# Kernel tuning notes

Measured on AMD Instinct MI355X. Metric: run time of the kernel, lower is better.

## Reference

```python
import jax, jax.numpy as jnp
import numpy as np

B, U, V, C = 2, 8, 512, 256
H, DK = 8, 64            # num_heads, key_query_features (per head)
R = 256                  # result_features; per-head value dim R//H = 32
CODE = 192
EPS = 1e-6               # affinity renorm epsilon
LN_EPS = 1e-5            # torch LayerNorm default
GAIN = 2.5               # post_attention_gain / post_mlp_gain buffers


def _ln(x, g, b):
    m = x.mean(-1, keepdims=True)
    v = ((x - m) ** 2).mean(-1, keepdims=True)
    return (x - m) / jnp.sqrt(v + LN_EPS) * g + b


def _modlin(x, c, W, Wc, b=None):
    # ModFC / ModLin: y = W(x * (1 + Wc c)) (+ b)
    y = (x * (1.0 + c @ Wc)) @ W
    return y if b is None else y + b


def setup_inputs() -> dict:
    key = jax.random.key(0)
    ks = jax.random.split(key, 16)
    s = 0.02
    return {
        'variables': jax.random.normal(ks[0], (B, U, V, C), jnp.float32),
        'codes': jax.random.normal(ks[1], (U, CODE), jnp.float32),
        'affinities': jax.random.uniform(ks[2], (B, U, V), jnp.float32),
        'ln1_g': jnp.ones((C,), jnp.float32),
        'ln1_b': jnp.zeros((C,), jnp.float32),
        'Wq': jax.random.normal(ks[3], (C, H * DK), jnp.float32) * s,
        'Wcq': jax.random.normal(ks[4], (CODE, C), jnp.float32) * s,
        'Wk': jax.random.normal(ks[5], (C, H * DK), jnp.float32) * s,
        'Wck': jax.random.normal(ks[6], (CODE, C), jnp.float32) * s,
        'Wv': jax.random.normal(ks[7], (C, R), jnp.float32) * s,
        'Wcv': jax.random.normal(ks[8], (CODE, C), jnp.float32) * s,
        'bv': jnp.zeros((R,), jnp.float32),
        'ln2_g': jnp.ones((R,), jnp.float32),
        'ln2_b': jnp.zeros((R,), jnp.float32),
        'W1': jax.random.normal(ks[9], (R, R), jnp.float32) * s,
        'Wc1': jax.random.normal(ks[10], (CODE, R), jnp.float32) * s,
        'b1m': jnp.zeros((R,), jnp.float32),
        'W2': jax.random.normal(ks[11], (R, R), jnp.float32) * s,
        'Wc2': jax.random.normal(ks[12], (CODE, R), jnp.float32) * s,
        'b2m': jnp.zeros((R,), jnp.float32),
    }


def reference(variables, codes, affinities, ln1_g, ln1_b, Wq, Wcq, Wk, Wck,
              Wv, Wcv, bv, ln2_g, ln2_b, W1, Wc1, b1m, W2, Wc2, b2m):
    # codes: [U, code] -> broadcast to [B, U, V, code]
    c4 = jnp.broadcast_to(codes[None, :, None, :], (B, U, V, CODE))
    xn = _ln(variables, ln1_g, ln1_b)                      # b u v c
    q = _modlin(xn, c4, Wq, Wcq).reshape(B, U, V, H, DK)   # b u v h d
    k = _modlin(xn, c4, Wk, Wck).reshape(B, U, V, H, DK)
    v = _modlin(xn, c4, Wv, Wcv, bv).reshape(B, U, V, H, R // H)
    # scores: b u r s h (attention over s); scale_attention_weights=False -> scale 1
    scores = jnp.einsum('burhd,bushd->bursh', q, k)
    dot = jax.nn.softmax(scores, axis=3)                   # softmax over s (dim=-2)
    # affinity modulation: aff_r * aff_s * weights, renormalized over s
    kmw = affinities[:, :, :, None, None] * affinities[:, :, None, :, None] * dot
    kmw = kmw / (kmw.sum(axis=3, keepdims=True) + EPS)
    att = jnp.einsum('bursh,bushc->burhc', kmw, v).reshape(B, U, V, R)
    g = affinities[..., None]
    # residual_mode='gating', variable_features==result_features
    attn_out = (1.0 - g) * variables + g * GAIN * att
    yn = _ln(attn_out, ln2_g, ln2_b)
    h1 = jax.nn.gelu(_modlin(yn, c4, W1, Wc1, b1m), approximate=False)
    h2 = jax.nn.gelu(_modlin(h1, c4, W2, Wc2, b2m), approximate=False)
    mlp_out = h2 * g
    results = (1.0 - g) * attn_out + g * GAIN * mlp_out
    return results
```

## Files before the change

kernel.cpp:

```cpp
#include <hip/hip_runtime.h>
#include <math.h>

#define B_ 2
#define U_ 8
#define V_ 512
#define C_ 256
#define H_ 8
#define R_ 256
#define EPS_ 1e-6f
#define LN_EPS_ 1e-5f
#define GAIN_ 2.5f

typedef __attribute__((ext_vector_type(8))) short bf16x8;
typedef __attribute__((ext_vector_type(4))) float f32x4;
typedef unsigned short ushort_t;

__device__ __forceinline__ ushort_t f2bf(float x) {
    union { float f; unsigned u; } v; v.f = x;
    unsigned r = v.u + 0x7fffu + ((v.u >> 16) & 1u);
    return (ushort_t)(r >> 16);
}

__device__ __forceinline__ float waveReduceSum(float v) {
    #pragma unroll
    for (int m = 1; m < 64; m <<= 1) v += __shfl_xor(v, m);
    return v;
}

__device__ __forceinline__ float gelu_exact(float x) {
    return 0.5f * x * (1.f + erff(x * 0.70710678118654752f));
}

__global__ __launch_bounds__(256) void k_prep(
    const float* __restrict__ codes,
    const float* __restrict__ Wcq, const float* __restrict__ Wck,
    const float* __restrict__ Wcv, const float* __restrict__ Wc1,
    const float* __restrict__ Wc2,
    const float* __restrict__ Wq, const float* __restrict__ Wk,
    const float* __restrict__ Wv, const float* __restrict__ W1,
    const float* __restrict__ W2,
    const float* __restrict__ x, const float* __restrict__ ln1g,
    const float* __restrict__ ln1b,
    ushort_t* __restrict__ wqkvT, ushort_t* __restrict__ w1T,
    ushort_t* __restrict__ w2T, ushort_t* __restrict__ xnb) {
    int bid = blockIdx.x;
    int tid = threadIdx.x;
    if (bid >= 896) {
        int row = (bid - 896) * 4 + (tid >> 6);
        int lane = tid & 63;
        const float* xr = x + (size_t)row * C_;
        float4 v = *(const float4*)&xr[lane * 4];
        float s = v.x + v.y + v.z + v.w;
        float ss = v.x * v.x + v.y * v.y + v.z * v.z + v.w * v.w;
        s = waveReduceSum(s); ss = waveReduceSum(ss);
        float mean = s * (1.f / 256.f);
        float var = ss * (1.f / 256.f) - mean * mean;
        float rstd = rsqrtf(var + LN_EPS_);
        float4 gg = *(const float4*)&ln1g[lane * 4];
        float4 bb = *(const float4*)&ln1b[lane * 4];
        unsigned lo = (unsigned)f2bf((v.x - mean) * rstd * gg.x + bb.x)
                    | ((unsigned)f2bf((v.y - mean) * rstd * gg.y + bb.y) << 16);
        unsigned hi = (unsigned)f2bf((v.z - mean) * rstd * gg.z + bb.z)
                    | ((unsigned)f2bf((v.w - mean) * rstd * gg.w + bb.w) << 16);
        uint2 pk; pk.x = lo; pk.y = hi;
        *(uint2*)&xnb[(size_t)row * C_ + lane * 4] = pk;
        return;
    }
    __shared__ float mpart[4][64];
    __shared__ float mrow[64];
    __shared__ ushort_t T[64][65];
    int id = bid;
    const float* W; int ldw, modIdx, colAdd, tilesPerU, base;
    ushort_t* dst; int dstCols;
    if (id < 256)      { base = 0;   W = Wq; ldw = 512; modIdx = 0; colAdd = 0;    dst = wqkvT; dstCols = 1280; tilesPerU = 32; }
    else if (id < 512) { base = 256; W = Wk; ldw = 512; modIdx = 1; colAdd = 512;  dst = wqkvT; dstCols = 1280; tilesPerU = 32; }
    else if (id < 640) { base = 512; W = Wv; ldw = 256; modIdx = 2; colAdd = 1024; dst = wqkvT; dstCols = 1280; tilesPerU = 16; }
    else if (id < 768) { base = 640; W = W1; ldw = 256; modIdx = 3; colAdd = 0;    dst = w1T;  dstCols = 256;  tilesPerU = 16; }
    else               { base = 768; W = W2; ldw = 256; modIdx = 4; colAdd = 0;    dst = w2T;  dstCols = 256;  tilesPerU = 16; }
    const float* Wc = (modIdx == 0) ? Wcq : (modIdx == 1) ? Wck :
                      (modIdx == 2) ? Wcv : (modIdx == 3) ? Wc1 : Wc2;
    int local = id - base;
    int u = local / tilesPerU;
    int t = local % tilesPerU;
    int nColTiles = ldw / 64;
    int c0 = (t / nColTiles) * 64;
    int col0 = (t % nColTiles) * 64;
    {
        const float* cd = codes + u * 192;
        int cc = tid & 63, g = tid >> 6;
        float accm = 0.f;
        #pragma unroll 4
        for (int jj = 0; jj < 48; ++jj) {
            int j = g * 48 + jj;
            accm = fmaf(cd[j], Wc[j * 256 + c0 + cc], accm);
        }
        mpart[g][cc] = accm;
        __syncthreads();
        if (tid < 64)
            mrow[tid] = 1.f + mpart[0][tid] + mpart[1][tid] + mpart[2][tid] + mpart[3][tid];
        __syncthreads();
    }
    int cl = tid >> 4;
    int cg = (tid & 15) * 4;
    #pragma unroll
    for (int it = 0; it < 4; ++it) {
        int c = cl + it * 16;
        float m = mrow[c];
        float4 wv = *(const float4*)&W[(size_t)(c0 + c) * ldw + col0 + cg];
        T[c][cg + 0] = f2bf(wv.x * m);
        T[c][cg + 1] = f2bf(wv.y * m);
        T[c][cg + 2] = f2bf(wv.z * m);
        T[c][cg + 3] = f2bf(wv.w * m);
    }
    __syncthreads();
    int j = tid >> 2;
    int ch = (tid & 3) * 16;
    ushort_t tmp[16];
    #pragma unroll
    for (int i = 0; i < 16; ++i) tmp[i] = T[ch + i][j];
    ushort_t* o = dst + ((size_t)u * dstCols + colAdd + col0 + j) * 256 + c0 + ch;
    *(bf16x8*)&o[0] = *(const bf16x8*)&tmp[0];
    *(bf16x8*)&o[8] = *(const bf16x8*)&tmp[8];
}

__global__ __launch_bounds__(256) void k_qkv(
    const ushort_t* __restrict__ X, const ushort_t* __restrict__ WT,
    const float* __restrict__ bv, ushort_t* __restrict__ out,
    ushort_t* __restrict__ vT) {
    __shared__ __align__(16) ushort_t xs[128][72];
    __shared__ __align__(16) ushort_t wt[128][72];
    int col0 = blockIdx.x * 128;
    int row0 = blockIdx.y * 128;
    int u = (row0 >> 9) & 7;
    const ushort_t* Wu = WT + (size_t)(u * 1280 + col0) * 256;
    int tid = threadIdx.x;
    int w = tid >> 6, l = tid & 63;
    int lr = l & 15, lg = l >> 4;
    int wm = w >> 1, wn = w & 1;
    f32x4 acc[4][4] = {};
    int sr = tid >> 3, sko = (tid & 7) * 8;
    for (int k0 = 0; k0 < 256; k0 += 64) {
        #pragma unroll
        for (int it = 0; it < 4; ++it) {
            int r = sr + it * 32;
            *(bf16x8*)&xs[r][sko] = *(const bf16x8*)&X[(size_t)(row0 + r) * 256 + k0 + sko];
            *(bf16x8*)&wt[r][sko] = *(const bf16x8*)&Wu[(size_t)r * 256 + k0 + sko];
        }
        __syncthreads();
        #pragma unroll
        for (int m = 0; m < 4; ++m) {
            #pragma unroll
            for (int kk = 0; kk < 2; ++kk) {
                bf16x8 a = *(const bf16x8*)&xs[wm * 64 + m * 16 + lr][kk * 32 + lg * 8];
                #pragma unroll
                for (int n = 0; n < 4; ++n) {
                    bf16x8 bb = *(const bf16x8*)&wt[wn * 64 + n * 16 + lr][kk * 32 + lg * 8];
                    acc[m][n] = __builtin_amdgcn_mfma_f32_16x16x32_bf16(a, bb, acc[m][n], 0, 0, 0);
                }
            }
        }
        __syncthreads();
    }
    #pragma unroll
    for (int m = 0; m < 4; ++m) {
        int rowb = row0 + wm * 64 + m * 16 + lg * 4;
        #pragma unroll
        for (int n = 0; n < 4; ++n) {
            int col = col0 + wn * 64 + n * 16 + lr;
            float bval = (col >= 1024) ? bv[col - 1024] : 0.f;
            ushort_t pk4[4];
            #pragma unroll
            for (int i = 0; i < 4; ++i) {
                float v = acc[m][n][i] + bval;
                pk4[i] = f2bf(v);
                out[(size_t)(rowb + i) * 1280 + col] = pk4[i];
            }
            if (col >= 1024) {
                int hh = (col - 1024) >> 5, cc = (col - 1024) & 31;
                int bu = rowb >> 9;
                uint2 pw;
                pw.x = (unsigned)pk4[0] | ((unsigned)pk4[1] << 16);
                pw.y = (unsigned)pk4[2] | ((unsigned)pk4[3] << 16);
                *(uint2*)&vT[(size_t)((bu * 8 + hh) * 32 + cc) * 512 + (rowb & 511)] = pw;
            }
        }
    }
}

__global__ __launch_bounds__(256) void k_attn(
    const ushort_t* __restrict__ qkv, const ushort_t* __restrict__ vT,
    const float* __restrict__ aff, float* __restrict__ att) {
    __shared__ __align__(16) ushort_t Qs[64][72];
    __shared__ __align__(16) ushort_t Ks[64][72];
    __shared__ __align__(16) ushort_t Pt[64][72];
    __shared__ __align__(16) ushort_t Vt[32][72];
    __shared__ float As[64];
    int id = blockIdx.x;
    int xcd = id & 7, sl = id >> 3;
    int bu = xcd + 8 * (sl >> 6);
    int inr = sl & 63;
    int h = inr & 7;
    int r0 = (inr >> 3) * 64;
    const ushort_t* base = qkv + (size_t)bu * 512 * 1280;
    const ushort_t* vbase = vT + (size_t)((bu * 8 + h) * 32) * 512;
    int tid = threadIdx.x;
    int w = tid >> 6, l = tid & 63;
    int lr = l & 15, lg = l >> 4;
    int sr = tid >> 3, sko = (tid & 7) * 8;
    *(bf16x8*)&Qs[sr][sko]      = *(const bf16x8*)&base[(size_t)(r0 + sr) * 1280 + h * 64 + sko];
    *(bf16x8*)&Qs[sr + 32][sko] = *(const bf16x8*)&base[(size_t)(r0 + sr + 32) * 1280 + h * 64 + sko];
    bf16x8 kr0 = *(const bf16x8*)&base[(size_t)sr * 1280 + 512 + h * 64 + sko];
    bf16x8 kr1 = *(const bf16x8*)&base[(size_t)(sr + 32) * 1280 + 512 + h * 64 + sko];
    bf16x8 vr  = *(const bf16x8*)&vbase[(size_t)sr * 512 + sko];
    float afv = (tid < 64) ? aff[bu * 512 + tid] : 0.f;
    *(bf16x8*)&Ks[sr][sko] = kr0;
    *(bf16x8*)&Ks[sr + 32][sko] = kr1;
    if (sr < 32) *(bf16x8*)&Vt[sr][sko] = vr;
    if (tid < 64) As[tid] = afv;
    __syncthreads();
    float wsum = 0.f, asum = 0.f;
    f32x4 pacc[2] = {};
    for (int t = 0; t < 8; ++t) {
        int s0n = (t + 1) * 64;
        if (t < 7) {
            kr0 = *(const bf16x8*)&base[(size_t)(s0n + sr) * 1280 + 512 + h * 64 + sko];
            kr1 = *(const bf16x8*)&base[(size_t)(s0n + sr + 32) * 1280 + 512 + h * 64 + sko];
            if (sr < 32) vr = *(const bf16x8*)&vbase[(size_t)sr * 512 + s0n + sko];
            if (tid < 64) afv = aff[bu * 512 + s0n + tid];
        }
        #pragma unroll
        for (int n = 0; n < 4; ++n) {
            f32x4 sc = {};
            #pragma unroll
            for (int kk = 0; kk < 2; ++kk) {
                bf16x8 ka = *(const bf16x8*)&Ks[n * 16 + lr][kk * 32 + lg * 8];
                bf16x8 qb = *(const bf16x8*)&Qs[w * 16 + lr][kk * 32 + lg * 8];
                sc = __builtin_amdgcn_mfma_f32_16x16x32_bf16(ka, qb, sc, 0, 0, 0);
            }
            float4 a4 = *(const float4*)&As[n * 16 + lg * 4];
            float e0 = __expf(sc[0]), e1 = __expf(sc[1]);
            float e2 = __expf(sc[2]), e3 = __expf(sc[3]);
            wsum += (e0 + e1) + (e2 + e3);
            float ae0 = e0 * a4.x, ae1 = e1 * a4.y, ae2 = e2 * a4.z, ae3 = e3 * a4.w;
            asum += (ae0 + ae1) + (ae2 + ae3);
            uint2 pw;
            pw.x = (unsigned)f2bf(ae0) | ((unsigned)f2bf(ae1) << 16);
            pw.y = (unsigned)f2bf(ae2) | ((unsigned)f2bf(ae3) << 16);
            *(uint2*)&Pt[w * 16 + lr][n * 16 + lg * 4] = pw;
        }
        #pragma unroll
        for (int n = 0; n < 2; ++n) {
            #pragma unroll
            for (int kk = 0; kk < 2; ++kk) {
                bf16x8 pa = *(const bf16x8*)&Pt[w * 16 + lr][kk * 32 + lg * 8];
                bf16x8 vb = *(const bf16x8*)&Vt[n * 16 + lr][kk * 32 + lg * 8];
                pacc[n] = __builtin_amdgcn_mfma_f32_16x16x32_bf16(pa, vb, pacc[n], 0, 0, 0);
            }
        }
        __syncthreads();
        if (t < 7) {
            *(bf16x8*)&Ks[sr][sko] = kr0;
            *(bf16x8*)&Ks[sr + 32][sko] = kr1;
            if (sr < 32) *(bf16x8*)&Vt[sr][sko] = vr;
            if (tid < 64) As[tid] = afv;
            __syncthreads();
        }
    }
    asum += __shfl_xor(asum, 16); asum += __shfl_xor(asum, 32);
    wsum += __shfl_xor(wsum, 16); wsum += __shfl_xor(wsum, 32);
    float ar = aff[bu * 512 + r0 + w * 16 + lr];
    float scale = ar / (ar * asum + EPS_ * wsum);
    #pragma unroll
    for (int i = 0; i < 4; ++i) {
        float sc_i = __shfl(scale, lg * 4 + i);
        int q = r0 + w * 16 + lg * 4 + i;
        float* ob = att + ((size_t)bu * 512 + q) * 256 + h * 32;
        ob[lr]      = pacc[0][i] * sc_i;
        ob[16 + lr] = pacc[1][i] * sc_i;
    }
}

__global__ __launch_bounds__(256) void k_tail(
    const float* __restrict__ x, const float* __restrict__ att,
    const float* __restrict__ aff, const float* __restrict__ g2,
    const float* __restrict__ b2, const ushort_t* __restrict__ w1T,
    const ushort_t* __restrict__ w2T, const float* __restrict__ b1m,
    const float* __restrict__ b2m, float* __restrict__ outp) {
    __shared__ __align__(16) ushort_t yn[32][264];
    __shared__ __align__(16) ushort_t wt[256][72];
    int r0 = blockIdx.x * 32;
    int u = (r0 >> 9) & 7;
    int tid = threadIdx.x;
    {
        int row = tid >> 3, cb = (tid & 7) * 32;
        float a = aff[r0 + row];
        const float* xr = x + (size_t)(r0 + row) * 256 + cb;
        const float* ar = att + (size_t)(r0 + row) * 256 + cb;
        float4 o[8];
        float s = 0.f, ss = 0.f;
        #pragma unroll
        for (int j = 0; j < 8; ++j) {
            float4 xv = *(const float4*)&xr[j * 4];
            float4 av = *(const float4*)&ar[j * 4];
            float4 t;
            t.x = (1.f - a) * xv.x + a * GAIN_ * av.x;
            t.y = (1.f - a) * xv.y + a * GAIN_ * av.y;
            t.z = (1.f - a) * xv.z + a * GAIN_ * av.z;
            t.w = (1.f - a) * xv.w + a * GAIN_ * av.w;
            o[j] = t;
            s += (t.x + t.y) + (t.z + t.w);
            ss += (t.x * t.x + t.y * t.y) + (t.z * t.z + t.w * t.w);
        }
        s += __shfl_xor(s, 1); s += __shfl_xor(s, 2); s += __shfl_xor(s, 4);
        ss += __shfl_xor(ss, 1); ss += __shfl_xor(ss, 2); ss += __shfl_xor(ss, 4);
        float mean = s * (1.f / 256.f);
        float var = ss * (1.f / 256.f) - mean * mean;
        float rstd = rsqrtf(var + LN_EPS_);
        #pragma unroll
        for (int j = 0; j < 8; ++j) {
            float4 gg = *(const float4*)&g2[cb + j * 4];
            float4 bb = *(const float4*)&b2[cb + j * 4];
            uint2 pk;
            pk.x = (unsigned)f2bf((o[j].x - mean) * rstd * gg.x + bb.x)
                 | ((unsigned)f2bf((o[j].y - mean) * rstd * gg.y + bb.y) << 16);
            pk.y = (unsigned)f2bf((o[j].z - mean) * rstd * gg.z + bb.z)
                 | ((unsigned)f2bf((o[j].w - mean) * rstd * gg.w + bb.w) << 16);
            *(uint2*)&yn[row][cb + j * 4] = pk;
        }
    }
    __syncthreads();
    int w = tid >> 6, l = tid & 63, lr = l & 15, lg = l >> 4;
    int tokT = w & 1, nh = w >> 1;
    int scol = tid >> 3, sko = (tid & 7) * 8;
    const ushort_t* W1u = w1T + (size_t)u * 256 * 256;
    const ushort_t* W2u = w2T + (size_t)u * 256 * 256;
    f32x4 acc[8] = {};
    for (int k0 = 0; k0 < 256; k0 += 64) {
        #pragma unroll
        for (int it = 0; it < 8; ++it)
            *(bf16x8*)&wt[scol + it * 32][sko] =
                *(const bf16x8*)&W1u[(size_t)(scol + it * 32) * 256 + k0 + sko];
        __syncthreads();
        #pragma unroll
        for (int n = 0; n < 8; ++n) {
            #pragma unroll
            for (int kk = 0; kk < 2; ++kk) {
                bf16x8 a = *(const bf16x8*)&wt[(nh * 8 + n) * 16 + lr][kk * 32 + lg * 8];
                bf16x8 b = *(const bf16x8*)&yn[tokT * 16 + lr][k0 + kk * 32 + lg * 8];
                acc[n] = __builtin_amdgcn_mfma_f32_16x16x32_bf16(a, b, acc[n], 0, 0, 0);
            }
        }
        __syncthreads();
    }
    #pragma unroll
    for (int n = 0; n < 8; ++n) {
        int nc = (nh * 8 + n) * 16 + lg * 4;
        float4 bv1 = *(const float4*)&b1m[nc];
        ushort_t p0 = f2bf(gelu_exact(acc[n][0] + bv1.x));
        ushort_t p1 = f2bf(gelu_exact(acc[n][1] + bv1.y));
        ushort_t p2 = f2bf(gelu_exact(acc[n][2] + bv1.z));
        ushort_t p3 = f2bf(gelu_exact(acc[n][3] + bv1.w));
        uint2 pw;
        pw.x = (unsigned)p0 | ((unsigned)p1 << 16);
        pw.y = (unsigned)p2 | ((unsigned)p3 << 16);
        *(uint2*)&yn[tokT * 16 + lr][nc] = pw;
    }
    f32x4 acc2[8] = {};
    for (int k0 = 0; k0 < 256; k0 += 64) {
        #pragma unroll
        for (int it = 0; it < 8; ++it)
            *(bf16x8*)&wt[scol + it * 32][sko] =
                *(const bf16x8*)&W2u[(size_t)(scol + it * 32) * 256 + k0 + sko];
        __syncthreads();
        #pragma unroll
        for (int n = 0; n < 8; ++n) {
            #pragma unroll
            for (int kk = 0; kk < 2; ++kk) {
                bf16x8 a = *(const bf16x8*)&wt[(nh * 8 + n) * 16 + lr][kk * 32 + lg * 8];
                bf16x8 b = *(const bf16x8*)&yn[tokT * 16 + lr][k0 + kk * 32 + lg * 8];
                acc2[n] = __builtin_amdgcn_mfma_f32_16x16x32_bf16(a, b, acc2[n], 0, 0, 0);
            }
        }
        __syncthreads();
    }
    int orow = r0 + tokT * 16 + lr;
    float a = aff[orow];
    #pragma unroll
    for (int n = 0; n < 8; ++n) {
        int nc = (nh * 8 + n) * 16 + lg * 4;
        float4 bv2 = *(const float4*)&b2m[nc];
        float4 xv = *(const float4*)&x[(size_t)orow * 256 + nc];
        float4 av = *(const float4*)&att[(size_t)orow * 256 + nc];
        float4 r;
        {
            float h2 = gelu_exact(acc2[n][0] + bv2.x);
            float ao = (1.f - a) * xv.x + a * GAIN_ * av.x;
            r.x = (1.f - a) * ao + GAIN_ * a * a * h2;
        }
        {
            float h2 = gelu_exact(acc2[n][1] + bv2.y);
            float ao = (1.f - a) * xv.y + a * GAIN_ * av.y;
            r.y = (1.f - a) * ao + GAIN_ * a * a * h2;
        }
        {
            float h2 = gelu_exact(acc2[n][2] + bv2.z);
            float ao = (1.f - a) * xv.z + a * GAIN_ * av.z;
            r.z = (1.f - a) * ao + GAIN_ * a * a * h2;
        }
        {
            float h2 = gelu_exact(acc2[n][3] + bv2.w);
            float ao = (1.f - a) * xv.w + a * GAIN_ * av.w;
            r.w = (1.f - a) * ao + GAIN_ * a * a * h2;
        }
        *(float4*)&outp[(size_t)orow * 256 + nc] = r;
    }
}

extern "C" void kernel_launch(void* const* d_in, const int* in_sizes, int n_in,
                              void* d_out, int out_size, void* d_ws, size_t ws_size,
                              hipStream_t stream) {
    const float* variables  = (const float*)d_in[0];
    const float* codes      = (const float*)d_in[1];
    const float* affinities = (const float*)d_in[2];
    const float* ln1_g = (const float*)d_in[3];
    const float* ln1_b = (const float*)d_in[4];
    const float* Wq  = (const float*)d_in[5];
    const float* Wcq = (const float*)d_in[6];
    const float* Wk  = (const float*)d_in[7];
    const float* Wck = (const float*)d_in[8];
    const float* Wv  = (const float*)d_in[9];
    const float* Wcv = (const float*)d_in[10];
    const float* bv  = (const float*)d_in[11];
    const float* ln2_g = (const float*)d_in[12];
    const float* ln2_b = (const float*)d_in[13];
    const float* W1  = (const float*)d_in[14];
    const float* Wc1 = (const float*)d_in[15];
    const float* b1m = (const float*)d_in[16];
    const float* W2  = (const float*)d_in[17];
    const float* Wc2 = (const float*)d_in[18];
    const float* b2m = (const float*)d_in[19];

    char* p = (char*)d_ws;
    float* attF     = (float*)p;    p += 8388608;
    ushort_t* xnb   = (ushort_t*)p; p += 4194304;
    ushort_t* wqkvT = (ushort_t*)p; p += 5242880;
    ushort_t* w1T   = (ushort_t*)p; p += 1048576;
    ushort_t* w2T   = (ushort_t*)p; p += 1048576;
    ushort_t* qkvb  = (ushort_t*)p; p += 20971520;
    ushort_t* vTb   = (ushort_t*)p; p += 4194304;
    float* outp = (float*)d_out;

    k_prep<<<2944, 256, 0, stream>>>(codes, Wcq, Wck, Wcv, Wc1, Wc2,
                                     Wq, Wk, Wv, W1, W2,
                                     variables, ln1_g, ln1_b,
                                     wqkvT, w1T, w2T, xnb);
    k_qkv<<<dim3(10, 64), 256, 0, stream>>>(xnb, wqkvT, bv, qkvb, vTb);
    k_attn<<<1024, 256, 0, stream>>>(qkvb, vTb, affinities, attF);
    k_tail<<<256, 256, 0, stream>>>(variables, attF, affinities, ln2_g, ln2_b,
                                    w1T, w2T, b1m, b2m, outp);
}
```

Baseline: 166.8 us.

## Prefetch QKV tiles in registers, stage V transpose via LDS, bf16 attention output

The QKV GEMM now prefetches the next K-slice into registers while computing the current one. The V-column epilogue is restaged through shared memory so the transposed V writes are coalesced 16-byte stores. The attention output is stored as bf16 instead of fp32, halving that intermediate's traffic, and k_tail is re-tiled to 16 rows per block with twice the blocks. k_tail also caches the residual attn_out in LDS instead of rereading x and att, and packed v_cvt_pk_bf16 conversions are used throughout. In exchange, storing attention output in bf16 lowers precision, and the smaller k_tail tiles reload each weight tile for half as many rows.

```diff
diff --git a/kernel.cpp b/kernel.cpp
--- a/kernel.cpp
+++ b/kernel.cpp
@@ -19,6 +19,16 @@
     union { float f; unsigned u; } v; v.f = x;
     unsigned r = v.u + 0x7fffu + ((v.u >> 16) & 1u);
     return (ushort_t)(r >> 16);
+}
+
+__device__ __forceinline__ float bf2f(ushort_t h) {
+    union { unsigned u; float f; } v; v.u = (unsigned)h << 16; return v.f;
+}
+
+__device__ __forceinline__ unsigned cvt_pk_bf16(float lo, float hi) {
+    unsigned r;
+    asm("v_cvt_pk_bf16_f32 %0, %1, %2" : "=v"(r) : "v"(lo), "v"(hi));
+    return r;
 }
 
 __device__ __forceinline__ float waveReduceSum(float v) {
@@ -58,11 +68,11 @@
         float rstd = rsqrtf(var + LN_EPS_);
         float4 gg = *(const float4*)&ln1g[lane * 4];
         float4 bb = *(const float4*)&ln1b[lane * 4];
-        unsigned lo = (unsigned)f2bf((v.x - mean) * rstd * gg.x + bb.x)
-                    | ((unsigned)f2bf((v.y - mean) * rstd * gg.y + bb.y) << 16);
-        unsigned hi = (unsigned)f2bf((v.z - mean) * rstd * gg.z + bb.z)
-                    | ((unsigned)f2bf((v.w - mean) * rstd * gg.w + bb.w) << 16);
-        uint2 pk; pk.x = lo; pk.y = hi;
+        uint2 pk;
+        pk.x = (unsigned)f2bf((v.x - mean) * rstd * gg.x + bb.x)
+             | ((unsigned)f2bf((v.y - mean) * rstd * gg.y + bb.y) << 16);
+        pk.y = (unsigned)f2bf((v.z - mean) * rstd * gg.z + bb.z)
+             | ((unsigned)f2bf((v.w - mean) * rstd * gg.w + bb.w) << 16);
         *(uint2*)&xnb[(size_t)row * C_ + lane * 4] = pk;
         return;
     }
@@ -127,8 +137,9 @@
     const ushort_t* __restrict__ X, const ushort_t* __restrict__ WT,
     const float* __restrict__ bv, ushort_t* __restrict__ out,
     ushort_t* __restrict__ vT) {
-    __shared__ __align__(16) ushort_t xs[128][72];
-    __shared__ __align__(16) ushort_t wt[128][72];
+    __shared__ __align__(16) ushort_t smem[2 * 128 * 72];
+    ushort_t (*xs)[72] = (ushort_t (*)[72])smem;
+    ushort_t (*wt)[72] = (ushort_t (*)[72])(smem + 128 * 72);
     int col0 = blockIdx.x * 128;
     int row0 = blockIdx.y * 128;
     int u = (row0 >> 9) & 7;
@@ -139,14 +150,27 @@
     int wm = w >> 1, wn = w & 1;
     f32x4 acc[4][4] = {};
     int sr = tid >> 3, sko = (tid & 7) * 8;
-    for (int k0 = 0; k0 < 256; k0 += 64) {
+    bf16x8 xr[4], wr[4];
+    #pragma unroll
+    for (int it = 0; it < 4; ++it) {
+        xr[it] = *(const bf16x8*)&X[(size_t)(row0 + sr + it * 32) * 256 + sko];
+        wr[it] = *(const bf16x8*)&Wu[(size_t)(sr + it * 32) * 256 + sko];
+    }
+    for (int t = 0; t < 4; ++t) {
         #pragma unroll
         for (int it = 0; it < 4; ++it) {
-            int r = sr + it * 32;
-            *(bf16x8*)&xs[r][sko] = *(const bf16x8*)&X[(size_t)(row0 + r) * 256 + k0 + sko];
-            *(bf16x8*)&wt[r][sko] = *(const bf16x8*)&Wu[(size_t)r * 256 + k0 + sko];
-        }
-        __syncthreads();
+            *(bf16x8*)&xs[sr + it * 32][sko] = xr[it];
+            *(bf16x8*)&wt[sr + it * 32][sko] = wr[it];
+        }
+        __syncthreads();
+        if (t < 3) {
+            int k0 = (t + 1) * 64;
+            #pragma unroll
+            for (int it = 0; it < 4; ++it) {
+                xr[it] = *(const bf16x8*)&X[(size_t)(row0 + sr + it * 32) * 256 + k0 + sko];
+                wr[it] = *(const bf16x8*)&Wu[(size_t)(sr + it * 32) * 256 + k0 + sko];
+            }
+        }
         #pragma unroll
         for (int m = 0; m < 4; ++m) {
             #pragma unroll
@@ -161,35 +185,49 @@
         }
         __syncthreads();
     }
-    #pragma unroll
-    for (int m = 0; m < 4; ++m) {
-        int rowb = row0 + wm * 64 + m * 16 + lg * 4;
+    if (col0 < 1024) {
+        #pragma unroll
+        for (int m = 0; m < 4; ++m) {
+            int rowb = row0 + wm * 64 + m * 16 + lg * 4;
+            #pragma unroll
+            for (int n = 0; n < 4; ++n) {
+                int col = col0 + wn * 64 + n * 16 + lr;
+                #pragma unroll
+                for (int i = 0; i < 4; ++i)
+                    out[(size_t)(rowb + i) * 1280 + col] = f2bf(acc[m][n][i]);
+            }
+        }
+    } else {
+        ushort_t (*vbuf)[136] = (ushort_t (*)[136])smem;
         #pragma unroll
         for (int n = 0; n < 4; ++n) {
-            int col = col0 + wn * 64 + n * 16 + lr;
-            float bval = (col >= 1024) ? bv[col - 1024] : 0.f;
-            ushort_t pk4[4];
-            #pragma unroll
-            for (int i = 0; i < 4; ++i) {
-                float v = acc[m][n][i] + bval;
-                pk4[i] = f2bf(v);
-                out[(size_t)(rowb + i) * 1280 + col] = pk4[i];
-            }
-            if (col >= 1024) {
-                int hh = (col - 1024) >> 5, cc = (col - 1024) & 31;
-                int bu = rowb >> 9;
+            int c = wn * 64 + n * 16 + lr;
+            float bval = bv[col0 - 1024 + c];
+            #pragma unroll
+            for (int m = 0; m < 4; ++m) {
+                int s = wm * 64 + m * 16 + lg * 4;
                 uint2 pw;
-                pw.x = (unsigned)pk4[0] | ((unsigned)pk4[1] << 16);
-                pw.y = (unsigned)pk4[2] | ((unsigned)pk4[3] << 16);
-                *(uint2*)&vT[(size_t)((bu * 8 + hh) * 32 + cc) * 512 + (rowb & 511)] = pw;
-            }
+                pw.x = cvt_pk_bf16(acc[m][n][0] + bval, acc[m][n][1] + bval);
+                pw.y = cvt_pk_bf16(acc[m][n][2] + bval, acc[m][n][3] + bval);
+                *(uint2*)&vbuf[c][s] = pw;
+            }
+        }
+        __syncthreads();
+        int bu = row0 >> 9;
+        size_t grow0 = (size_t)(bu * 256 + (col0 - 1024));
+        int srow = row0 & 511;
+        int cc = tid >> 4, so = (tid & 15) * 8;
+        #pragma unroll
+        for (int it = 0; it < 8; ++it) {
+            int c = cc + it * 16;
+            *(bf16x8*)&vT[(grow0 + c) * 512 + srow + so] = *(const bf16x8*)&vbuf[c][so];
         }
     }
 }
 
 __global__ __launch_bounds__(256) void k_attn(
     const ushort_t* __restrict__ qkv, const ushort_t* __restrict__ vT,
-    const float* __restrict__ aff, float* __restrict__ att) {
+    const float* __restrict__ aff, ushort_t* __restrict__ attB) {
     __shared__ __align__(16) ushort_t Qs[64][72];
     __shared__ __align__(16) ushort_t Ks[64][72];
     __shared__ __align__(16) ushort_t Pt[64][72];
@@ -244,8 +282,8 @@
             float ae0 = e0 * a4.x, ae1 = e1 * a4.y, ae2 = e2 * a4.z, ae3 = e3 * a4.w;
             asum += (ae0 + ae1) + (ae2 + ae3);
             uint2 pw;
-            pw.x = (unsigned)f2bf(ae0) | ((unsigned)f2bf(ae1) << 16);
-            pw.y = (unsigned)f2bf(ae2) | ((unsigned)f2bf(ae3) << 16);
+            pw.x = cvt_pk_bf16(ae0, ae1);
+            pw.y = cvt_pk_bf16(ae2, ae3);
             *(uint2*)&Pt[w * 16 + lr][n * 16 + lg * 4] = pw;
         }
         #pragma unroll
@@ -274,67 +312,65 @@
     for (int i = 0; i < 4; ++i) {
         float sc_i = __shfl(scale, lg * 4 + i);
         int q = r0 + w * 16 + lg * 4 + i;
-        float* ob = att + ((size_t)bu * 512 + q) * 256 + h * 32;
-        ob[lr]      = pacc[0][i] * sc_i;
-        ob[16 + lr] = pacc[1][i] * sc_i;
+        ushort_t* ob = attB + ((size_t)bu * 512 + q) * 256 + h * 32;
+        ob[lr]      = f2bf(pacc[0][i] * sc_i);
+        ob[16 + lr] = f2bf(pacc[1][i] * sc_i);
     }
 }
 
 __global__ __launch_bounds__(256) void k_tail(
-    const float* __restrict__ x, const float* __restrict__ att,
+    const float* __restrict__ x, const ushort_t* __restrict__ attB,
     const float* __restrict__ aff, const float* __restrict__ g2,
     const float* __restrict__ b2, const ushort_t* __restrict__ w1T,
     const ushort_t* __restrict__ w2T, const float* __restrict__ b1m,
     const float* __restrict__ b2m, float* __restrict__ outp) {
-    __shared__ __align__(16) ushort_t yn[32][264];
+    __shared__ __align__(16) ushort_t ynL[16][264];
+    __shared__ __align__(16) float aoL[16][260];
     __shared__ __align__(16) ushort_t wt[256][72];
-    int r0 = blockIdx.x * 32;
+    int r0 = blockIdx.x * 16;
     int u = (r0 >> 9) & 7;
     int tid = threadIdx.x;
     {
-        int row = tid >> 3, cb = (tid & 7) * 32;
+        int row = tid >> 4, cb = (tid & 15) * 16;
         float a = aff[r0 + row];
         const float* xr = x + (size_t)(r0 + row) * 256 + cb;
-        const float* ar = att + (size_t)(r0 + row) * 256 + cb;
-        float4 o[8];
+        const ushort_t* ar = attB + (size_t)(r0 + row) * 256 + cb;
+        ushort_t av[16];
+        *(bf16x8*)&av[0] = *(const bf16x8*)&ar[0];
+        *(bf16x8*)&av[8] = *(const bf16x8*)&ar[8];
+        float o[16];
         float s = 0.f, ss = 0.f;
         #pragma unroll
-        for (int j = 0; j < 8; ++j) {
-            float4 xv = *(const float4*)&xr[j * 4];
-            float4 av = *(const float4*)&ar[j * 4];
-            float4 t;
-            t.x = (1.f - a) * xv.x + a * GAIN_ * av.x;
-            t.y = (1.f - a) * xv.y + a * GAIN_ * av.y;
-            t.z = (1.f - a) * xv.z + a * GAIN_ * av.z;
-            t.w = (1.f - a) * xv.w + a * GAIN_ * av.w;
-            o[j] = t;
-            s += (t.x + t.y) + (t.z + t.w);
-            ss += (t.x * t.x + t.y * t.y) + (t.z * t.z + t.w * t.w);
-        }
-        s += __shfl_xor(s, 1); s += __shfl_xor(s, 2); s += __shfl_xor(s, 4);
-        ss += __shfl_xor(ss, 1); ss += __shfl_xor(ss, 2); ss += __shfl_xor(ss, 4);
+        for (int j = 0; j < 16; ++j) {
+            float t = (1.f - a) * xr[j] + a * GAIN_ * bf2f(av[j]);
+            o[j] = t; s += t; ss += t * t;
+        }
+        s += __shfl_xor(s, 1); s += __shfl_xor(s, 2);
+        s += __shfl_xor(s, 4); s += __shfl_xor(s, 8);
+        ss += __shfl_xor(ss, 1); ss += __shfl_xor(ss, 2);
+        ss += __shfl_xor(ss, 4); ss += __shfl_xor(ss, 8);
         float mean = s * (1.f / 256.f);
         float var = ss * (1.f / 256.f) - mean * mean;
         float rstd = rsqrtf(var + LN_EPS_);
         #pragma unroll
-        for (int j = 0; j < 8; ++j) {
-            float4 gg = *(const float4*)&g2[cb + j * 4];
-            float4 bb = *(const float4*)&b2[cb + j * 4];
+        for (int j = 0; j < 16; j += 4) {
+            float4 gg = *(const float4*)&g2[cb + j];
+            float4 bb = *(const float4*)&b2[cb + j];
+            *(float4*)&aoL[row][cb + j] = make_float4(o[j], o[j+1], o[j+2], o[j+3]);
             uint2 pk;
-            pk.x = (unsigned)f2bf((o[j].x - mean) * rstd * gg.x + bb.x)
-                 | ((unsigned)f2bf((o[j].y - mean) * rstd * gg.y + bb.y) << 16);
-            pk.y = (unsigned)f2bf((o[j].z - mean) * rstd * gg.z + bb.z)
-                 | ((unsigned)f2bf((o[j].w - mean) * rstd * gg.w + bb.w) << 16);
-            *(uint2*)&yn[row][cb + j * 4] = pk;
+            pk.x = cvt_pk_bf16((o[j]   - mean) * rstd * gg.x + bb.x,
+                               (o[j+1] - mean) * rstd * gg.y + bb.y);
+            pk.y = cvt_pk_bf16((o[j+2] - mean) * rstd * gg.z + bb.z,
+                               (o[j+3] - mean) * rstd * gg.w + bb.w);
+            *(uint2*)&ynL[row][cb + j] = pk;
         }
     }
     __syncthreads();
     int w = tid >> 6, l = tid & 63, lr = l & 15, lg = l >> 4;
-    int tokT = w & 1, nh = w >> 1;
     int scol = tid >> 3, sko = (tid & 7) * 8;
-    const ushort_t* W1u = w1T + (size_t)u * 256 * 256;
-    const ushort_t* W2u = w2T + (size_t)u * 256 * 256;
-    f32x4 acc[8] = {};
+    const ushort_t* W1u = w1T + (size_t)u * 65536;
+    const ushort_t* W2u = w2T + (size_t)u * 65536;
+    f32x4 acc[4] = {};
     for (int k0 = 0; k0 < 256; k0 += 64) {
         #pragma unroll
         for (int it = 0; it < 8; ++it)
@@ -342,30 +378,27 @@
                 *(const bf16x8*)&W1u[(size_t)(scol + it * 32) * 256 + k0 + sko];
         __syncthreads();
         #pragma unroll
-        for (int n = 0; n < 8; ++n) {
+        for (int n = 0; n < 4; ++n) {
             #pragma unroll
             for (int kk = 0; kk < 2; ++kk) {
-                bf16x8 a = *(const bf16x8*)&wt[(nh * 8 + n) * 16 + lr][kk * 32 + lg * 8];
-                bf16x8 b = *(const bf16x8*)&yn[tokT * 16 + lr][k0 + kk * 32 + lg * 8];
+                bf16x8 a = *(const bf16x8*)&wt[w * 64 + n * 16 + lr][kk * 32 + lg * 8];
+                bf16x8 b = *(const bf16x8*)&ynL[lr][k0 + kk * 32 + lg * 8];
                 acc[n] = __builtin_amdgcn_mfma_f32_16x16x32_bf16(a, b, acc[n], 0, 0, 0);
             }
         }
         __syncthreads();
     }
     #pragma unroll
-    for (int n = 0; n < 8; ++n) {
-        int nc = (nh * 8 + n) * 16 + lg * 4;
+    for (int n = 0; n < 4; ++n) {
+        int nc = w * 64 + n * 16 + lg * 4;
         float4 bv1 = *(const float4*)&b1m[nc];
-        ushort_t p0 = f2bf(gelu_exact(acc[n][0] + bv1.x));
-        ushort_t p1 = f2bf(gelu_exact(acc[n][1] + bv1.y));
-        ushort_t p2 = f2bf(gelu_exact(acc[n][2] + bv1.z));
-        ushort_t p3 = f2bf(gelu_exact(acc[n][3] + bv1.w));
         uint2 pw;
-        pw.x = (unsigned)p0 | ((unsigned)p1 << 16);
-        pw.y = (unsigned)p2 | ((unsigned)p3 << 16);
-        *(uint2*)&yn[tokT * 16 + lr][nc] = pw;
-    }
-    f32x4 acc2[8] = {};
+        pw.x = cvt_pk_bf16(gelu_exact(acc[n][0] + bv1.x), gelu_exact(acc[n][1] + bv1.y));
+        pw.y = cvt_pk_bf16(gelu_exact(acc[n][2] + bv1.z), gelu_exact(acc[n][3] + bv1.w));
+        *(uint2*)&ynL[lr][nc] = pw;
+    }
+    __syncthreads();
+    f32x4 acc2[4] = {};
     for (int k0 = 0; k0 < 256; k0 += 64) {
         #pragma unroll
         for (int it = 0; it < 8; ++it)
@@ -373,44 +406,38 @@
                 *(const bf16x8*)&W2u[(size_t)(scol + it * 32) * 256 + k0 + sko];
         __syncthreads();
         #pragma unroll
-        for (int n = 0; n < 8; ++n) {
+        for (int n = 0; n < 4; ++n) {
             #pragma unroll
             for (int kk = 0; kk < 2; ++kk) {
-                bf16x8 a = *(const bf16x8*)&wt[(nh * 8 + n) * 16 + lr][kk * 32 + lg * 8];
-                bf16x8 b = *(const bf16x8*)&yn[tokT * 16 + lr][k0 + kk * 32 + lg * 8];
+                bf16x8 a = *(const bf16x8*)&wt[w * 64 + n * 16 + lr][kk * 32 + lg * 8];
+                bf16x8 b = *(const bf16x8*)&ynL[lr][k0 + kk * 32 + lg * 8];
                 acc2[n] = __builtin_amdgcn_mfma_f32_16x16x32_bf16(a, b, acc2[n], 0, 0, 0);
             }
         }
         __syncthreads();
     }
-    int orow = r0 + tokT * 16 + lr;
+    int orow = r0 + lr;
     float a = aff[orow];
     #pragma unroll
-    for (int n = 0; n < 8; ++n) {
-        int nc = (nh * 8 + n) * 16 + lg * 4;
+    for (int n = 0; n < 4; ++n) {
+        int nc = w * 64 + n * 16 + lg * 4;
         float4 bv2 = *(const float4*)&b2m[nc];
-        float4 xv = *(const float4*)&x[(size_t)orow * 256 + nc];
-        float4 av = *(const float4*)&att[(size_t)orow * 256 + nc];
         float4 r;
         {
             float h2 = gelu_exact(acc2[n][0] + bv2.x);
-            float ao = (1.f - a) * xv.x + a * GAIN_ * av.x;
-            r.x = (1.f - a) * ao + GAIN_ * a * a * h2;
+            r.x = (1.f - a) * aoL[lr][nc + 0] + GAIN_ * a * a * h2;
         }
         {
             float h2 = gelu_exact(acc2[n][1] + bv2.y);
-            float ao = (1.f - a) * xv.y + a * GAIN_ * av.y;
-            r.y = (1.f - a) * ao + GAIN_ * a * a * h2;
+            r.y = (1.f - a) * aoL[lr][nc + 1] + GAIN_ * a * a * h2;
         }
         {
             float h2 = gelu_exact(acc2[n][2] + bv2.z);
-            float ao = (1.f - a) * xv.z + a * GAIN_ * av.z;
-            r.z = (1.f - a) * ao + GAIN_ * a * a * h2;
+            r.z = (1.f - a) * aoL[lr][nc + 2] + GAIN_ * a * a * h2;
         }
         {
             float h2 = gelu_exact(acc2[n][3] + bv2.w);
-            float ao = (1.f - a) * xv.w + a * GAIN_ * av.w;
-            r.w = (1.f - a) * ao + GAIN_ * a * a * h2;
+            r.w = (1.f - a) * aoL[lr][nc + 3] + GAIN_ * a * a * h2;
         }
         *(float4*)&outp[(size_t)orow * 256 + nc] = r;
     }
@@ -441,7 +468,7 @@
     const float* b2m = (const float*)d_in[19];
 
     char* p = (char*)d_ws;
-    float* attF     = (float*)p;    p += 8388608;
+    ushort_t* attB  = (ushort_t*)p; p += 4194304;
     ushort_t* xnb   = (ushort_t*)p; p += 4194304;
     ushort_t* wqkvT = (ushort_t*)p; p += 5242880;
     ushort_t* w1T   = (ushort_t*)p; p += 1048576;
@@ -455,7 +482,7 @@
                                      variables, ln1_g, ln1_b,
                                      wqkvT, w1T, w2T, xnb);
     k_qkv<<<dim3(10, 64), 256, 0, stream>>>(xnb, wqkvT, bv, qkvb, vTb);
-    k_attn<<<1024, 256, 0, stream>>>(qkvb, vTb, affinities, attF);
-    k_tail<<<256, 256, 0, stream>>>(variables, attF, affinities, ln2_g, ln2_b,
+    k_attn<<<1024, 256, 0, stream>>>(qkvb, vTb, affinities, attB);
+    k_tail<<<512, 256, 0, stream>>>(variables, attB, affinities, ln2_g, ln2_b,
                                     w1T, w2T, b1m, b2m, outp);
 }
```

Result: faster. 150.9 us (-9.5%).
